# Performance work log

Measured on AMD Instinct MI355X. Metric: run time of the kernel, lower is better.

## Reference

```python
import jax, jax.numpy as jnp
import numpy as np
from jax import lax

PATCH_SIZE = 7
NEIGH_SIZE = 9
SIGMA = 2.0
EPS = 1e-05


def _gaussian_kernel(sigma, sz):
    mid = sz // 2
    ax = np.arange(sz) - mid
    g = np.exp(-(ax[:, None] ** 2 + ax[None, :] ** 2) / (2.0 * sigma ** 2)) / (2.0 * np.pi * sigma ** 2)
    return g.astype(np.float32)


KERNEL = jnp.asarray(_gaussian_kernel(SIGMA, PATCH_SIZE))[None, None]  # (1,1,7,7)

_half = NEIGH_SIZE // 2
SHIFTS = jnp.asarray(
    [(x, y) for x in range(-_half, NEIGH_SIZE - _half)
     for y in range(-_half, NEIGH_SIZE - _half) if (x, y) != (0, 0)],
    dtype=jnp.int32)  # (80, 2) — xshift outer loop, yshift inner, matching torch order
SHIFTS4 = jnp.asarray([(-1, 0), (1, 0), (0, -1), (0, 1)], dtype=jnp.int32)


def _translate(img, tx, ty):
    # Faithful to torch affine_grid + grid_sample(nearest, zeros, align_corners=False):
    # a 'translation' of tx in normalized coords samples input at pixel j + tx*W/2.
    # H, W even and tx, ty integers -> exact integer pixel shifts, zero padding.
    H, W = img.shape
    px = jnp.arange(W) + tx * (W // 2)
    py = jnp.arange(H) + ty * (H // 2)
    mask = ((py >= 0) & (py < H))[:, None] & ((px >= 0) & (px < W))[None, :]
    out = img[jnp.clip(py, 0, H - 1)[:, None], jnp.clip(px, 0, W - 1)[None, :]]
    return jnp.where(mask, out, jnp.zeros((), img.dtype))


def _blur(x):
    # x: (N, H, W); conv2d with gaussian kernel, stride 1, padding 3 (same for 7x7)
    y = lax.conv_general_dilated(x[:, None], KERNEL, (1, 1), [(3, 3), (3, 3)],
                                 dimension_numbers=('NCHW', 'OIHW', 'NCHW'))
    return y[:, 0]


def _dp_batch(img2d, shifts):
    # Dp for a batch of shifts: shift, diff, square, gaussian blur
    shifted = jax.vmap(lambda s: _translate(img2d, s[0], s[1]))(shifts)  # (N,H,W)
    return _blur((img2d[None] - shifted) ** 2)


def setup_inputs() -> dict:
    key = jax.random.key(0)
    k1, k2 = jax.random.split(key)
    image1 = jax.random.normal(k1, (1, 1, 1024, 1024), dtype=jnp.float32)
    image2 = jax.random.normal(k2, (1, 1, 1024, 1024), dtype=jnp.float32)
    return {"image1": image1, "image2": image2}


def reference(image1, image2):
    img1 = image1[0, 0]  # (H, W)
    img2 = image2[0, 0]
    H, W = img1.shape
    reduce_size = (PATCH_SIZE + NEIGH_SIZE - 2) // 2  # = 7
    # Vimg: average of 4 single-pixel-neighborhood Dp's on image1, + eps
    Vimg = _dp_batch(img1, SHIFTS4).sum(axis=0) / 4.0 + EPS  # (H, W)
    # 80-shift MIND responses on image2
    D2 = _dp_batch(img2, SHIFTS)  # (80, H, W)
    mind = jnp.exp(-D2 / Vimg[None])
    # torch slices: dim1 end index is (C - reduce_size) = 1-7 = -6 -> H-6;
    # dim2 end index is (H - reduce_size). Replicated exactly (H == W).
    out = mind[:, reduce_size:H + 1 - reduce_size, reduce_size:H - reduce_size]
    mx = jnp.max(out, axis=0)
    return jnp.mean(out / mx[None])
```

## Files before the change

kernel.cpp:

```cpp
#include <hip/hip_runtime.h>
#include <cmath>

#define IMG_W 1024
#define NT    128
#define OC    (NT - 6)
#define ROWS  12
#define STEPS (ROWS + 6)
#define PADW  (NT + 6)

struct GK { float gh[7]; float gv[7]; };

__global__ __launch_bounds__(NT)
void mind_sweep(const float* __restrict__ img1, const float* __restrict__ img2,
                float* __restrict__ out, GK gk)
{
    __shared__ float4 buf[2][PADW];

    const int tx = (int)threadIdx.x;
    const int X0 = 7 + (int)blockIdx.x * OC;
    const int Y0 = 7 + (int)blockIdx.y * ROWS;

    const int sx_raw = X0 - 3 + tx;
    const int sx  = min(sx_raw, 1023);
    const int sxp = sx ^ 512;
    const bool xok = (tx >= 3) && (tx <= NT - 4) && (sx_raw <= 1016);

    float glx[7], ghx[7];
    #pragma unroll
    for (int kx = 0; kx < 7; ++kx) {
        const bool lo = (((sx_raw + kx - 3) & 512) == 0);
        glx[kx] = lo ? gk.gh[kx] : 0.f;
        ghx[kx] = lo ? 0.f : gk.gh[kx];
    }

    float wHlo[7] = {0}, wHhi[7] = {0}, wV[7] = {0},
          wDlo[7] = {0}, wDhi[7] = {0}, wU[7] = {0};
    float tsum = 0.f;

    #pragma unroll
    for (int s = 0; s < STEPS; ++s) {
        const int sr  = min(Y0 - 3 + s, 1023);
        const int srp = sr ^ 512;
        const float* __restrict__ r2  = img2 + sr  * IMG_W;
        const float* __restrict__ r2p = img2 + srp * IMG_W;
        const float* __restrict__ r1  = img1 + sr  * IMG_W;
        const float* __restrict__ r1p = img1 + srp * IMG_W;
        const float a  = r2[sx], b = r2[sxp], c = r2p[sx], d = r2p[sxp];
        const float u  = r1[sx], ub = r1[sxp], uc = r1p[sx];
        const float a2 = a * a;
        const float tb = a - b, tc = a - c, td = a - d;
        const float su = u - ub, sv = u - uc;
        float4 f;
        f.x = fmaf(tb, tb, -a2);
        f.y = fmaf(tc, tc, -a2);
        f.z = fmaf(td, td, -a2);
        f.w = fmaf(u, u + u, fmaf(su, su, sv * sv));
        buf[s & 1][tx + 3] = f;
        __syncthreads();

        float hHlo = 0, hHhi = 0, hV = 0, hDlo = 0, hDhi = 0, hU = 0;
        #pragma unroll
        for (int kx = 0; kx < 7; ++kx) {
            const float4 g = buf[s & 1][tx + kx];
            hHlo = fmaf(glx[kx],  g.x, hHlo);
            hHhi = fmaf(ghx[kx],  g.x, hHhi);
            hV   = fmaf(gk.gh[kx], g.y, hV);
            hDlo = fmaf(glx[kx],  g.z, hDlo);
            hDhi = fmaf(ghx[kx],  g.z, hDhi);
            hU   = fmaf(gk.gh[kx], g.w, hU);
        }
        #pragma unroll
        for (int i = 0; i < 6; ++i) {
            wHlo[i] = wHlo[i+1]; wHhi[i] = wHhi[i+1]; wV[i] = wV[i+1];
            wDlo[i] = wDlo[i+1]; wDhi[i] = wDhi[i+1]; wU[i] = wU[i+1];
        }
        wHlo[6] = hHlo; wHhi[6] = hHhi; wV[6] = hV;
        wDlo[6] = hDlo; wDhi[6] = hDhi; wU[6] = hU;

        if (s >= 6) {
            const int y = Y0 + s - 6;
            if (y <= 1017) {
                float Ph=0,Qh=0,Pv=0,Qv=0,Ppp=0,Ppm=0,Pmp=0,Pmm=0,V4=0;
                #pragma unroll
                for (int ky = 0; ky < 7; ++ky) {
                    const float g = gk.gv[ky];
                    const bool ylo = (((y - 3 + ky) & 512) == 0);
                    const float wl = ylo ? g : 0.f;
                    const float wh = ylo ? 0.f : g;
                    Ph  = fmaf(g,  wHlo[ky], Ph);
                    Qh  = fmaf(g,  wHhi[ky], Qh);
                    Pv  = fmaf(wl, wV[ky],   Pv);
                    Qv  = fmaf(wh, wV[ky],   Qv);
                    Ppp = fmaf(wl, wDlo[ky], Ppp);
                    Ppm = fmaf(wh, wDlo[ky], Ppm);
                    Pmp = fmaf(wl, wDhi[ky], Pmp);
                    Pmm = fmaf(wh, wDhi[ky], Pmm);
                    V4  = fmaf(g,  wU[ky],   V4);
                }
                const float V = fmaf(V4, 0.25f, 1e-5f);
                const float invV = 1.0f / V;
                float M = fminf(0.f, Ph);
                M = fminf(M, Qh);  M = fminf(M, Pv);  M = fminf(M, Qv);
                M = fminf(M, Ppp); M = fminf(M, Pmp); M = fminf(M, Ppm); M = fminf(M, Pmm);
                const float pix = 72.f * __expf(M * invV)
                    + __expf((M - Ph ) * invV) + __expf((M - Qh ) * invV)
                    + __expf((M - Pv ) * invV) + __expf((M - Qv ) * invV)
                    + __expf((M - Ppp) * invV) + __expf((M - Pmp) * invV)
                    + __expf((M - Ppm) * invV) + __expf((M - Pmm) * invV);
                tsum += xok ? pix : 0.f;
            }
        }
    }

    #pragma unroll
    for (int off = 32; off > 0; off >>= 1)
        tsum += __shfl_down(tsum, off, 64);
    __shared__ float wsum[2];
    __syncthreads();
    if ((tx & 63) == 0) wsum[tx >> 6] = tsum;
    __syncthreads();
    if (tx == 0)
        atomicAdd(out, (wsum[0] + wsum[1]) * (1.0f / 81688800.0f));
}

extern "C" void kernel_launch(void* const* d_in, const int* in_sizes, int n_in,
                              void* d_out, int out_size, void* d_ws, size_t ws_size,
                              hipStream_t stream) {
    const float* img1 = (const float*)d_in[0];
    const float* img2 = (const float*)d_in[1];
    float* out = (float*)d_out;

    GK gk;
    for (int i = 0; i < 7; ++i) {
        const double d = i - 3;
        gk.gh[i] = (float)std::exp(-(d * d) / 8.0);
        gk.gv[i] = (float)(std::exp(-(d * d) / 8.0) / (8.0 * M_PI));
    }

    hipMemsetAsync(d_out, 0, sizeof(float), stream);
    dim3 block(NT, 1);
    dim3 grid(9, 85);
    mind_sweep<<<grid, block, 0, stream>>>(img1, img2, out, gk);
}
```

Before: 83.98 us.

## Use single-wavefront blocks with wave barriers instead of block syncs

Result: slower. 99.48 us (+18.5%).

```diff
diff --git a/kernel.cpp b/kernel.cpp
--- a/kernel.cpp
+++ b/kernel.cpp
@@ -2,33 +2,31 @@
 #include <cmath>
 
 #define IMG_W 1024
-#define NT    128
-#define OC    (NT - 6)
-#define ROWS  12
-#define STEPS (ROWS + 6)
-#define PADW  (NT + 6)
+#define RROWS 8
+#define STEPS (RROWS + 6)
+#define OCW   58
 
 struct GK { float gh[7]; float gv[7]; };
 
-__global__ __launch_bounds__(NT)
-void mind_sweep(const float* __restrict__ img1, const float* __restrict__ img2,
-                float* __restrict__ out, GK gk)
+__global__ __launch_bounds__(64)
+void mind_wave(const float* __restrict__ img1, const float* __restrict__ img2,
+               float* __restrict__ out, GK gk)
 {
-    __shared__ float4 buf[2][PADW];
+    __shared__ float4 buf[72];
 
-    const int tx = (int)threadIdx.x;
-    const int X0 = 7 + (int)blockIdx.x * OC;
-    const int Y0 = 7 + (int)blockIdx.y * ROWS;
+    const int lane = (int)threadIdx.x;
+    const int X0 = 4 + OCW * (int)blockIdx.x;
+    const int Y0 = 7 + RROWS * (int)blockIdx.y;
 
-    const int sx_raw = X0 - 3 + tx;
-    const int sx  = min(sx_raw, 1023);
+    const int sxr = X0 + lane;
+    const int sx  = min(sxr, 1023);
     const int sxp = sx ^ 512;
-    const bool xok = (tx >= 3) && (tx <= NT - 4) && (sx_raw <= 1016);
+    const bool xok = (lane >= 3) && (lane <= 60) && (sxr <= 1016);
 
     float glx[7], ghx[7];
     #pragma unroll
     for (int kx = 0; kx < 7; ++kx) {
-        const bool lo = (((sx_raw + kx - 3) & 512) == 0);
+        const bool lo = (((sxr + kx - 3) & 512) == 0);
         glx[kx] = lo ? gk.gh[kx] : 0.f;
         ghx[kx] = lo ? 0.f : gk.gh[kx];
     }
@@ -45,8 +43,8 @@
         const float* __restrict__ r2p = img2 + srp * IMG_W;
         const float* __restrict__ r1  = img1 + sr  * IMG_W;
         const float* __restrict__ r1p = img1 + srp * IMG_W;
-        const float a  = r2[sx], b = r2[sxp], c = r2p[sx], d = r2p[sxp];
-        const float u  = r1[sx], ub = r1[sxp], uc = r1p[sx];
+        const float a = r2[sx], b = r2[sxp], c = r2p[sx], d = r2p[sxp];
+        const float u = r1[sx], ub = r1[sxp], uc = r1p[sx];
         const float a2 = a * a;
         const float tb = a - b, tc = a - c, td = a - d;
         const float su = u - ub, sv = u - uc;
@@ -55,20 +53,22 @@
         f.y = fmaf(tc, tc, -a2);
         f.z = fmaf(td, td, -a2);
         f.w = fmaf(u, u + u, fmaf(su, su, sv * sv));
-        buf[s & 1][tx + 3] = f;
-        __syncthreads();
+        buf[lane + 3] = f;
+        __builtin_amdgcn_wave_barrier();
 
         float hHlo = 0, hHhi = 0, hV = 0, hDlo = 0, hDhi = 0, hU = 0;
         #pragma unroll
         for (int kx = 0; kx < 7; ++kx) {
-            const float4 g = buf[s & 1][tx + kx];
-            hHlo = fmaf(glx[kx],  g.x, hHlo);
-            hHhi = fmaf(ghx[kx],  g.x, hHhi);
+            const float4 g = buf[lane + kx];
+            hHlo = fmaf(glx[kx],   g.x, hHlo);
+            hHhi = fmaf(ghx[kx],   g.x, hHhi);
             hV   = fmaf(gk.gh[kx], g.y, hV);
-            hDlo = fmaf(glx[kx],  g.z, hDlo);
-            hDhi = fmaf(ghx[kx],  g.z, hDhi);
+            hDlo = fmaf(glx[kx],   g.z, hDlo);
+            hDhi = fmaf(ghx[kx],   g.z, hDhi);
             hU   = fmaf(gk.gh[kx], g.w, hU);
         }
+        __builtin_amdgcn_wave_barrier();
+
         #pragma unroll
         for (int i = 0; i < 6; ++i) {
             wHlo[i] = wHlo[i+1]; wHhi[i] = wHhi[i+1]; wV[i] = wV[i+1];
@@ -115,12 +115,8 @@
     #pragma unroll
     for (int off = 32; off > 0; off >>= 1)
         tsum += __shfl_down(tsum, off, 64);
-    __shared__ float wsum[2];
-    __syncthreads();
-    if ((tx & 63) == 0) wsum[tx >> 6] = tsum;
-    __syncthreads();
-    if (tx == 0)
-        atomicAdd(out, (wsum[0] + wsum[1]) * (1.0f / 81688800.0f));
+    if (lane == 0)
+        atomicAdd(out, tsum * (1.0f / 81688800.0f));
 }
 
 extern "C" void kernel_launch(void* const* d_in, const int* in_sizes, int n_in,
@@ -138,7 +134,7 @@
     }
 
     hipMemsetAsync(d_out, 0, sizeof(float), stream);
-    dim3 block(NT, 1);
-    dim3 grid(9, 85);
-    mind_sweep<<<grid, block, 0, stream>>>(img1, img2, out, gk);
+    dim3 block(64, 1);
+    dim3 grid(18, 127);
+    mind_wave<<<grid, block, 0, stream>>>(img1, img2, out, gk);
 }
```
